# Optimization experiments

Measured on AMD Instinct MI355X. Metric: run time of the kernel, lower is better.

The kernel has to match this reference:

```python
import jax, jax.numpy as jnp
import numpy as np

EMBED_DIM = 1024
NUM_HEADS = 16
HEAD_DIM = EMBED_DIM // NUM_HEADS
B, S = 8, 1024


def setup_inputs() -> dict:
    key = jax.random.key(0)
    ks = jax.random.split(key, 8)
    scale = 1.0 / np.sqrt(EMBED_DIM)
    return {
        "q": jax.random.normal(ks[0], (B, S, EMBED_DIM), jnp.float32),
        "v": jax.random.normal(ks[1], (B, S, EMBED_DIM), jnp.float32),
        "Wq": jax.random.normal(ks[2], (EMBED_DIM, EMBED_DIM), jnp.float32) * scale,
        "bq": jnp.zeros((EMBED_DIM,), jnp.float32),
        "Wk": jax.random.normal(ks[3], (EMBED_DIM, EMBED_DIM), jnp.float32) * scale,
        "bk": jnp.zeros((EMBED_DIM,), jnp.float32),
        "Wv": jax.random.normal(ks[4], (EMBED_DIM, EMBED_DIM), jnp.float32) * scale,
        "bv": jnp.zeros((EMBED_DIM,), jnp.float32),
    }


def reference(q, v, Wq, bq, Wk, bk, Wv, bv):
    # call(q, v, k=None): k defaults to v, then compute_multihead_attention(q, v, k)
    # maps (q_arg=q, k_arg=v, v_arg=v) in self-attention.
    qp = q @ Wq + bq                     # [B, S, E]
    kp = v @ Wk + bk                     # [B, S, E]
    vp = v @ Wv + bv                     # [B, S, E]
    # split along feature dim into heads (same math as tf.split+concat on batch)
    qh = qp.reshape(B, S, NUM_HEADS, HEAD_DIM)
    kh = kp.reshape(B, S, NUM_HEADS, HEAD_DIM)
    vh = vp.reshape(B, S, NUM_HEADS, HEAD_DIM)
    # NOTE: original scales by 1/sqrt(embed_dim), not 1/sqrt(head_dim)
    scores = jnp.einsum("bqhd,bkhd->bhqk", qh, kh) / np.sqrt(EMBED_DIM)
    att = jax.nn.softmax(scores, axis=-1)
    out = jnp.einsum("bhqk,bkhd->bqhd", att, vh)  # [B, S, H, Dh]
    return out.reshape(B, S, EMBED_DIM)
```

## Files before the change

kernel.cpp:

```cpp
#include <hip/hip_runtime.h>
#include <cstdint>
#include <cstddef>

#define E 1024
#define S 1024
#define NB 8
#define NH 16
#define DH 64

typedef __bf16 bf16_t;
typedef __bf16 bf16x8 __attribute__((ext_vector_type(8)));
typedef __bf16 bf16x4 __attribute__((ext_vector_type(4)));
typedef __bf16 bf16x2 __attribute__((ext_vector_type(2)));
typedef short s16x4 __attribute__((ext_vector_type(4)));
typedef float f32x4 __attribute__((ext_vector_type(4)));

static __device__ __forceinline__ void gload_lds16(const void* g, void* l) {
  __builtin_amdgcn_global_load_lds((const __attribute__((address_space(1))) void*)g,
                                   (__attribute__((address_space(3))) void*)l, 16, 0, 0);
}

static __device__ __forceinline__ float fast_exp2(float x) {
#if __has_builtin(__builtin_amdgcn_exp2f)
  return __builtin_amdgcn_exp2f(x);
#else
  float r;
  asm("v_exp_f32 %0, %1" : "=v"(r) : "v"(x));
  return r;
#endif
}

__global__ __launch_bounds__(256) void convert_kernel(
    const float* __restrict__ q, const float* __restrict__ v,
    bf16_t* __restrict__ qb, bf16_t* __restrict__ vb) {
  const float* src = blockIdx.y ? v : q;
  bf16_t* dst = blockIdx.y ? vb : qb;
  const size_t i = ((size_t)blockIdx.x * 256 + threadIdx.x) * 8;
  float4 a = *(const float4*)(src + i);
  float4 b = *(const float4*)(src + i + 4);
  bf16x8 o = {(bf16_t)a.x, (bf16_t)a.y, (bf16_t)a.z, (bf16_t)a.w,
              (bf16_t)b.x, (bf16_t)b.y, (bf16_t)b.z, (bf16_t)b.w};
  *(bf16x8*)(dst + i) = o;
}

__global__ void wtrans_kernel(const float* __restrict__ Wq, const float* __restrict__ Wk,
                              const float* __restrict__ Wv, bf16_t* __restrict__ Wqt,
                              bf16_t* __restrict__ Wkt, bf16_t* __restrict__ Wvt) {
  const float* W = (blockIdx.z == 0) ? Wq : (blockIdx.z == 1) ? Wk : Wv;
  bf16_t* Wt = (blockIdx.z == 0) ? Wqt : (blockIdx.z == 1) ? Wkt : Wvt;
  __shared__ float tile[32][33];
  const int n0 = blockIdx.x * 32, k0 = blockIdx.y * 32;
  const int tx = threadIdx.x, ty = threadIdx.y;
#pragma unroll
  for (int i = ty; i < 32; i += 8)
    tile[i][tx] = W[(size_t)(k0 + i) * E + n0 + tx];
  __syncthreads();
#pragma unroll
  for (int i = ty; i < 32; i += 8)
    Wt[(size_t)(n0 + i) * E + k0 + tx] = (bf16_t)tile[tx][i];
}

__global__ __launch_bounds__(256) void gemm_fused_kernel(
    const bf16_t* __restrict__ qbf, const bf16_t* __restrict__ vbf,
    const bf16_t* __restrict__ Wqt, const bf16_t* __restrict__ Wkt,
    const bf16_t* __restrict__ Wvt, const float* __restrict__ bq,
    const float* __restrict__ bk, const float* __restrict__ bv,
    bf16_t* __restrict__ qp, bf16_t* __restrict__ kp, bf16_t* __restrict__ vp,
    float qscale) {
  __shared__ bf16_t As[128 * 32];
  __shared__ bf16_t Bs[128 * 32];
  const int t = threadIdx.x;
  const int l = t & 63, w = t >> 6;
  const int lc = l & 15, lg = l >> 4;
  const int wm = (w >> 1) * 64, wn = (w & 1) * 64;

  const int nb = blockIdx.y;
  const int sel = nb >> 3;
  const bf16_t* A = sel ? vbf : qbf;
  const bf16_t* Bt = (sel == 0) ? Wqt : (sel == 1) ? Wkt : Wvt;
  const float* bias = (sel == 0) ? bq : (sel == 1) ? bk : bv;
  bf16_t* C = (sel == 0) ? qp : (sel == 1) ? kp : vp;
  const float scale = (sel == 0) ? qscale : 1.0f;

  const int m0 = blockIdx.x * 128;
  const int n0 = (nb & 7) * 128;

  const bf16_t* asrc = A + (size_t)(m0 + (t >> 2)) * E + (t & 3) * 8;
  const bf16_t* bsrc = Bt + (size_t)(n0 + (t >> 2)) * E + (t & 3) * 8;
  char* asd0 = (char*)As + w * 1024;
  char* bsd0 = (char*)Bs + w * 1024;

  f32x4 acc[4][4] = {};

  for (int k0 = 0; k0 < E; k0 += 32) {
    __syncthreads();
    gload_lds16(asrc + k0, asd0);
    gload_lds16(asrc + 64 * E + k0, asd0 + 4096);
    gload_lds16(bsrc + k0, bsd0);
    gload_lds16(bsrc + 64 * E + k0, bsd0 + 4096);
    __syncthreads();

    bf16x8 af[4], bf[4];
#pragma unroll
    for (int mi = 0; mi < 4; ++mi)
      af[mi] = *(const bf16x8*)&As[(wm + mi * 16 + lc) * 32 + lg * 8];
#pragma unroll
    for (int ni = 0; ni < 4; ++ni)
      bf[ni] = *(const bf16x8*)&Bs[(wn + ni * 16 + lc) * 32 + lg * 8];
#pragma unroll
    for (int mi = 0; mi < 4; ++mi)
#pragma unroll
      for (int ni = 0; ni < 4; ++ni)
        acc[mi][ni] = __builtin_amdgcn_mfma_f32_16x16x32_bf16(af[mi], bf[ni], acc[mi][ni], 0, 0, 0);
  }

#pragma unroll
  for (int ni = 0; ni < 4; ++ni) {
    const int n = n0 + wn + ni * 16 + lc;
    const float bv_ = bias[n];
#pragma unroll
    for (int mi = 0; mi < 4; ++mi) {
#pragma unroll
      for (int r = 0; r < 4; ++r) {
        const int m = m0 + wm + mi * 16 + lg * 4 + r;
        C[(size_t)m * E + n] = (bf16_t)((acc[mi][ni][r] + bv_) * scale);
      }
    }
  }
}

#if __has_builtin(__builtin_amdgcn_mfma_f32_16x16x16bf16_1k)
static __device__ __forceinline__ f32x4 mfma16(s16x4 a, s16x4 b, f32x4 c) {
  return __builtin_amdgcn_mfma_f32_16x16x16bf16_1k(a, b, c, 0, 0, 0);
}
#else
static __device__ __forceinline__ f32x4 mfma16(s16x4 a, s16x4 b, f32x4 c) {
  asm volatile("v_mfma_f32_16x16x16_bf16 %0, %1, %2, %0" : "+v"(c) : "v"(a), "v"(b));
  return c;
}
#endif

__global__ __launch_bounds__(256, 2) void attn_kernel(
    const bf16_t* __restrict__ qp, const bf16_t* __restrict__ kp,
    const bf16_t* __restrict__ vp, float* __restrict__ out) {
  __shared__ __align__(16) unsigned char KsB[2][64 * 128];
  __shared__ bf16_t Vs[2][64][72];
  const int t = threadIdx.x;
  const int w = t >> 6, l = t & 63;
  const int lc = l & 15, lg = l >> 4;

  const int swz = (blockIdx.x & 7) * 64 + (blockIdx.x >> 3);
  const int qblk = swz & 3, bh = swz >> 2;
  const int h = bh & 15, b = bh >> 4;
  const int qbase = qblk * 256 + w * 64;
  const size_t bh_off = (size_t)b * S * E + (size_t)h * DH;

  bf16x8 qf[4][2];
#pragma unroll
  for (int qi = 0; qi < 4; ++qi)
#pragma unroll
    for (int kc = 0; kc < 2; ++kc)
      qf[qi][kc] = *(const bf16x8*)(qp + bh_off + (size_t)(qbase + 16 * qi + lc) * E + kc * 32 + lg * 8);

  f32x4 po[4][4] = {};
  float l_[4] = {0.f, 0.f, 0.f, 0.f};

  const int krow = t >> 2, kc4 = t & 3;
  const int vkv2 = (t & 31) * 2, vd0 = (t >> 5) * 8;
  const bf16_t* kbase = kp + bh_off;
  const bf16_t* vbase = vp + bh_off;
  const int ksw = (krow & 7) << 4;

  bf16x8 ka0, ka1, va0, va1;
  {
    const bf16_t* ks = kbase + (size_t)krow * E + kc4 * 16;
    ka0 = *(const bf16x8*)ks;
    ka1 = *(const bf16x8*)(ks + 8);
    const bf16_t* vs = vbase + (size_t)vkv2 * E + vd0;
    va0 = *(const bf16x8*)vs;
    va1 = *(const bf16x8*)(vs + E);
    *(bf16x8*)&KsB[0][krow * 128 + ((kc4 * 32) ^ ksw)] = ka0;
    *(bf16x8*)&KsB[0][krow * 128 + ((kc4 * 32 + 16) ^ ksw)] = ka1;
#pragma unroll
    for (int j = 0; j < 8; ++j) {
      bf16x2 pr;
      pr[0] = va0[j];
      pr[1] = va1[j];
      *(bf16x2*)&Vs[0][vd0 + j][vkv2] = pr;
    }
  }
  int cur = 0;

  for (int kv0 = 0; kv0 < S; kv0 += 64) {
    __syncthreads();

    const bool more = (kv0 + 64 < S);
    if (more) {
      const bf16_t* ks = kbase + (size_t)(kv0 + 64 + krow) * E + kc4 * 16;
      ka0 = *(const bf16x8*)ks;
      ka1 = *(const bf16x8*)(ks + 8);
      const bf16_t* vs = vbase + (size_t)(kv0 + 64 + vkv2) * E + vd0;
      va0 = *(const bf16x8*)vs;
      va1 = *(const bf16x8*)(vs + E);
    }

    s16x4 pa[4][4];
    __builtin_amdgcn_s_setprio(1);
#pragma unroll
    for (int kvb = 0; kvb < 4; ++kvb) {
      const int row = kvb * 16 + lc;
      const int sw = (lc & 7) << 4;
      bf16x8 ak0 = *(const bf16x8*)&KsB[cur][row * 128 + ((lg * 16) ^ sw)];
      bf16x8 ak1 = *(const bf16x8*)&KsB[cur][row * 128 + ((64 + lg * 16) ^ sw)];
      f32x4 sc[4] = {};
#pragma unroll
      for (int qi = 0; qi < 4; ++qi) {
        sc[qi] = __builtin_amdgcn_mfma_f32_16x16x32_bf16(ak0, qf[qi][0], sc[qi], 0, 0, 0);
        sc[qi] = __builtin_amdgcn_mfma_f32_16x16x32_bf16(ak1, qf[qi][1], sc[qi], 0, 0, 0);
      }
#pragma unroll
      for (int qi = 0; qi < 4; ++qi) {
        const float e0 = fast_exp2(sc[qi][0]);
        const float e1 = fast_exp2(sc[qi][1]);
        const float e2 = fast_exp2(sc[qi][2]);
        const float e3 = fast_exp2(sc[qi][3]);
        l_[qi] += (e0 + e1) + (e2 + e3);
        bf16x4 pb = {(bf16_t)e0, (bf16_t)e1, (bf16_t)e2, (bf16_t)e3};
        pa[qi][kvb] = *(s16x4*)&pb;
      }
    }

#pragma unroll
    for (int ki = 0; ki < 4; ++ki) {
      s16x4 av[4];
#pragma unroll
      for (int ni = 0; ni < 4; ++ni)
        av[ni] = *(const s16x4*)&Vs[cur][16 * ni + lc][16 * ki + lg * 4];
#pragma unroll
      for (int qi = 0; qi < 4; ++qi)
#pragma unroll
        for (int ni = 0; ni < 4; ++ni)
          po[qi][ni] = mfma16(av[ni], pa[qi][ki], po[qi][ni]);
    }
    __builtin_amdgcn_s_setprio(0);

    if (more) {
      const int nb_ = cur ^ 1;
      *(bf16x8*)&KsB[nb_][krow * 128 + ((kc4 * 32) ^ ksw)] = ka0;
      *(bf16x8*)&KsB[nb_][krow * 128 + ((kc4 * 32 + 16) ^ ksw)] = ka1;
#pragma unroll
      for (int j = 0; j < 8; ++j) {
        bf16x2 pr;
        pr[0] = va0[j];
        pr[1] = va1[j];
        *(bf16x2*)&Vs[nb_][vd0 + j][vkv2] = pr;
      }
      cur = nb_;
    }
  }

#pragma unroll
  for (int qi = 0; qi < 4; ++qi) {
    float lt = l_[qi];
    lt += __shfl_xor(lt, 16, 64);
    lt += __shfl_xor(lt, 32, 64);
    const float inv = 1.0f / lt;
    const int qrow = qbase + 16 * qi + lc;
    float* op = out + (size_t)b * S * E + (size_t)qrow * E + h * DH;
#pragma unroll
    for (int ni = 0; ni < 4; ++ni) {
      f32x4 r = po[qi][ni] * inv;
      *(f32x4*)(op + 16 * ni + lg * 4) = r;
    }
  }
}

extern "C" void kernel_launch(void* const* d_in, const int* in_sizes, int n_in,
                              void* d_out, int out_size, void* d_ws, size_t ws_size,
                              hipStream_t stream) {
  const float* q  = (const float*)d_in[0];
  const float* v  = (const float*)d_in[1];
  const float* Wq = (const float*)d_in[2];
  const float* bq = (const float*)d_in[3];
  const float* Wk = (const float*)d_in[4];
  const float* bk = (const float*)d_in[5];
  const float* Wv = (const float*)d_in[6];
  const float* bv = (const float*)d_in[7];
  float* out = (float*)d_out;

  char* ws = (char*)d_ws;
  bf16_t* Wqt = (bf16_t*)(ws);
  bf16_t* Wkt = (bf16_t*)(ws + (size_t)2 * 1024 * 1024);
  bf16_t* Wvt = (bf16_t*)(ws + (size_t)4 * 1024 * 1024);
  bf16_t* qp  = (bf16_t*)(ws + (size_t)6 * 1024 * 1024);
  bf16_t* kp  = (bf16_t*)(ws + (size_t)22 * 1024 * 1024);
  bf16_t* vp  = (bf16_t*)(ws + (size_t)38 * 1024 * 1024);

  bf16_t* qbf = (bf16_t*)d_out;
  bf16_t* vbf = qbf + (size_t)NB * S * E;

  convert_kernel<<<dim3(4096, 2), 256, 0, stream>>>(q, v, qbf, vbf);
  wtrans_kernel<<<dim3(32, 32, 3), dim3(32, 8), 0, stream>>>(Wq, Wk, Wv, Wqt, Wkt, Wvt);

  const float qscale = 0.03125f * 1.44269504088896f;
  gemm_fused_kernel<<<dim3(64, 24), 256, 0, stream>>>(qbf, vbf, Wqt, Wkt, Wvt,
                                                      bq, bk, bv, qp, kp, vp, qscale);
  attn_kernel<<<dim3(512), 256, 0, stream>>>(qp, kp, vp, out);
}
```

Baseline: 139.1 us.

## Fuse fp32-to-bf16 input conversion into projection GEMM with register-prefetched A

```diff
diff --git a/kernel.cpp b/kernel.cpp
--- a/kernel.cpp
+++ b/kernel.cpp
@@ -30,19 +30,6 @@
 #endif
 }
 
-__global__ __launch_bounds__(256) void convert_kernel(
-    const float* __restrict__ q, const float* __restrict__ v,
-    bf16_t* __restrict__ qb, bf16_t* __restrict__ vb) {
-  const float* src = blockIdx.y ? v : q;
-  bf16_t* dst = blockIdx.y ? vb : qb;
-  const size_t i = ((size_t)blockIdx.x * 256 + threadIdx.x) * 8;
-  float4 a = *(const float4*)(src + i);
-  float4 b = *(const float4*)(src + i + 4);
-  bf16x8 o = {(bf16_t)a.x, (bf16_t)a.y, (bf16_t)a.z, (bf16_t)a.w,
-              (bf16_t)b.x, (bf16_t)b.y, (bf16_t)b.z, (bf16_t)b.w};
-  *(bf16x8*)(dst + i) = o;
-}
-
 __global__ void wtrans_kernel(const float* __restrict__ Wq, const float* __restrict__ Wk,
                               const float* __restrict__ Wv, bf16_t* __restrict__ Wqt,
                               bf16_t* __restrict__ Wkt, bf16_t* __restrict__ Wvt) {
@@ -61,13 +48,12 @@
 }
 
 __global__ __launch_bounds__(256) void gemm_fused_kernel(
-    const bf16_t* __restrict__ qbf, const bf16_t* __restrict__ vbf,
+    const float* __restrict__ qf32, const float* __restrict__ vf32,
     const bf16_t* __restrict__ Wqt, const bf16_t* __restrict__ Wkt,
     const bf16_t* __restrict__ Wvt, const float* __restrict__ bq,
     const float* __restrict__ bk, const float* __restrict__ bv,
     bf16_t* __restrict__ qp, bf16_t* __restrict__ kp, bf16_t* __restrict__ vp,
     float qscale) {
-  __shared__ bf16_t As[128 * 32];
   __shared__ bf16_t Bs[128 * 32];
   const int t = threadIdx.x;
   const int l = t & 63, w = t >> 6;
@@ -76,7 +62,7 @@
 
   const int nb = blockIdx.y;
   const int sel = nb >> 3;
-  const bf16_t* A = sel ? vbf : qbf;
+  const float* A = sel ? vf32 : qf32;
   const bf16_t* Bt = (sel == 0) ? Wqt : (sel == 1) ? Wkt : Wvt;
   const float* bias = (sel == 0) ? bq : (sel == 1) ? bk : bv;
   bf16_t* C = (sel == 0) ? qp : (sel == 1) ? kp : vp;
@@ -85,34 +71,64 @@
   const int m0 = blockIdx.x * 128;
   const int n0 = (nb & 7) * 128;
 
-  const bf16_t* asrc = A + (size_t)(m0 + (t >> 2)) * E + (t & 3) * 8;
+  const float* arow = A + (size_t)(m0 + wm + lc) * E + lg * 8;
   const bf16_t* bsrc = Bt + (size_t)(n0 + (t >> 2)) * E + (t & 3) * 8;
-  char* asd0 = (char*)As + w * 1024;
   char* bsd0 = (char*)Bs + w * 1024;
 
   f32x4 acc[4][4] = {};
 
-  for (int k0 = 0; k0 < E; k0 += 32) {
-    __syncthreads();
-    gload_lds16(asrc + k0, asd0);
-    gload_lds16(asrc + 64 * E + k0, asd0 + 4096);
+#define LOAD_A(dst, kk)                                   \
+  _Pragma("unroll") for (int mi = 0; mi < 4; ++mi) {      \
+    const float* p_ = arow + (size_t)mi * 16 * E + (kk);  \
+    dst[mi][0] = *(const f32x4*)p_;                       \
+    dst[mi][1] = *(const f32x4*)(p_ + 4);                 \
+  }
+
+#define CVT_A(dst, src)                                                        \
+  _Pragma("unroll") for (int mi = 0; mi < 4; ++mi) {                           \
+    dst[mi] = (bf16x8){(bf16_t)src[mi][0][0], (bf16_t)src[mi][0][1],           \
+                       (bf16_t)src[mi][0][2], (bf16_t)src[mi][0][3],           \
+                       (bf16_t)src[mi][1][0], (bf16_t)src[mi][1][1],           \
+                       (bf16_t)src[mi][1][2], (bf16_t)src[mi][1][3]};          \
+  }
+
+#define DO_MFMA(af_)                                                           \
+  {                                                                            \
+    bf16x8 bf_[4];                                                             \
+    _Pragma("unroll") for (int ni = 0; ni < 4; ++ni)                           \
+      bf_[ni] = *(const bf16x8*)&Bs[(wn + ni * 16 + lc) * 32 + lg * 8];        \
+    _Pragma("unroll") for (int mi = 0; mi < 4; ++mi)                           \
+      _Pragma("unroll") for (int ni = 0; ni < 4; ++ni)                         \
+        acc[mi][ni] =                                                          \
+            __builtin_amdgcn_mfma_f32_16x16x32_bf16(af_[mi], bf_[ni],          \
+                                                    acc[mi][ni], 0, 0, 0);     \
+  }
+
+  f32x4 aA[4][2], aB[4][2];
+  LOAD_A(aA, 0);
+
+  for (int k0 = 0; k0 < E; k0 += 64) {
+    __syncthreads();
     gload_lds16(bsrc + k0, bsd0);
     gload_lds16(bsrc + 64 * E + k0, bsd0 + 4096);
-    __syncthreads();
-
-    bf16x8 af[4], bf[4];
-#pragma unroll
-    for (int mi = 0; mi < 4; ++mi)
-      af[mi] = *(const bf16x8*)&As[(wm + mi * 16 + lc) * 32 + lg * 8];
-#pragma unroll
-    for (int ni = 0; ni < 4; ++ni)
-      bf[ni] = *(const bf16x8*)&Bs[(wn + ni * 16 + lc) * 32 + lg * 8];
-#pragma unroll
-    for (int mi = 0; mi < 4; ++mi)
-#pragma unroll
-      for (int ni = 0; ni < 4; ++ni)
-        acc[mi][ni] = __builtin_amdgcn_mfma_f32_16x16x32_bf16(af[mi], bf[ni], acc[mi][ni], 0, 0, 0);
-  }
+    LOAD_A(aB, k0 + 32);
+    bf16x8 af0[4];
+    CVT_A(af0, aA);
+    __syncthreads();
+    DO_MFMA(af0);
+
+    __syncthreads();
+    gload_lds16(bsrc + k0 + 32, bsd0);
+    gload_lds16(bsrc + 64 * E + k0 + 32, bsd0 + 4096);
+    if (k0 + 64 < E) LOAD_A(aA, k0 + 64);
+    bf16x8 af1[4];
+    CVT_A(af1, aB);
+    __syncthreads();
+    DO_MFMA(af1);
+  }
+#undef LOAD_A
+#undef CVT_A
+#undef DO_MFMA
 
 #pragma unroll
   for (int ni = 0; ni < 4; ++ni) {
@@ -296,14 +312,10 @@
   bf16_t* kp  = (bf16_t*)(ws + (size_t)22 * 1024 * 1024);
   bf16_t* vp  = (bf16_t*)(ws + (size_t)38 * 1024 * 1024);
 
-  bf16_t* qbf = (bf16_t*)d_out;
-  bf16_t* vbf = qbf + (size_t)NB * S * E;
-
-  convert_kernel<<<dim3(4096, 2), 256, 0, stream>>>(q, v, qbf, vbf);
   wtrans_kernel<<<dim3(32, 32, 3), dim3(32, 8), 0, stream>>>(Wq, Wk, Wv, Wqt, Wkt, Wvt);
 
   const float qscale = 0.03125f * 1.44269504088896f;
-  gemm_fused_kernel<<<dim3(64, 24), 256, 0, stream>>>(qbf, vbf, Wqt, Wkt, Wvt,
+  gemm_fused_kernel<<<dim3(64, 24), 256, 0, stream>>>(q, v, Wqt, Wkt, Wvt,
                                                       bq, bk, bv, qp, kp, vp, qscale);
   attn_kernel<<<dim3(512), 256, 0, stream>>>(qp, kp, vp, out);
 }
```

New measurement: 257.0 us. 84.8% more time.

## Rewrite QKV projection GEMM with 256x256 tiles, double-buffered LDS and swizzle

Applied to the files above, without the earlier changes.

```diff
diff --git a/kernel.cpp b/kernel.cpp
--- a/kernel.cpp
+++ b/kernel.cpp
@@ -60,69 +60,133 @@
     Wt[(size_t)(n0 + i) * E + k0 + tx] = (bf16_t)tile[tx][i];
 }
 
-__global__ __launch_bounds__(256) void gemm_fused_kernel(
+__global__ __launch_bounds__(512, 2) void gemm8_kernel(
     const bf16_t* __restrict__ qbf, const bf16_t* __restrict__ vbf,
     const bf16_t* __restrict__ Wqt, const bf16_t* __restrict__ Wkt,
     const bf16_t* __restrict__ Wvt, const float* __restrict__ bq,
     const float* __restrict__ bk, const float* __restrict__ bv,
     bf16_t* __restrict__ qp, bf16_t* __restrict__ kp, bf16_t* __restrict__ vp,
     float qscale) {
-  __shared__ bf16_t As[128 * 32];
-  __shared__ bf16_t Bs[128 * 32];
+  extern __shared__ __align__(16) char smem[];
+
   const int t = threadIdx.x;
-  const int l = t & 63, w = t >> 6;
+  const int wv = t >> 6, l = t & 63;
   const int lc = l & 15, lg = l >> 4;
-  const int wm = (w >> 1) * 64, wn = (w & 1) * 64;
-
-  const int nb = blockIdx.y;
-  const int sel = nb >> 3;
+  const int wr = wv >> 2, wc = wv & 3;
+
+  const int nt = blockIdx.y;
+  const int sel = nt >> 2;
   const bf16_t* A = sel ? vbf : qbf;
   const bf16_t* Bt = (sel == 0) ? Wqt : (sel == 1) ? Wkt : Wvt;
   const float* bias = (sel == 0) ? bq : (sel == 1) ? bk : bv;
   bf16_t* C = (sel == 0) ? qp : (sel == 1) ? kp : vp;
   const float scale = (sel == 0) ? qscale : 1.0f;
 
-  const int m0 = blockIdx.x * 128;
-  const int n0 = (nb & 7) * 128;
-
-  const bf16_t* asrc = A + (size_t)(m0 + (t >> 2)) * E + (t & 3) * 8;
-  const bf16_t* bsrc = Bt + (size_t)(n0 + (t >> 2)) * E + (t & 3) * 8;
-  char* asd0 = (char*)As + w * 1024;
-  char* bsd0 = (char*)Bs + w * 1024;
-
-  f32x4 acc[4][4] = {};
-
-  for (int k0 = 0; k0 < E; k0 += 32) {
-    __syncthreads();
-    gload_lds16(asrc + k0, asd0);
-    gload_lds16(asrc + 64 * E + k0, asd0 + 4096);
-    gload_lds16(bsrc + k0, bsd0);
-    gload_lds16(bsrc + 64 * E + k0, bsd0 + 4096);
-    __syncthreads();
-
-    bf16x8 af[4], bf[4];
-#pragma unroll
-    for (int mi = 0; mi < 4; ++mi)
-      af[mi] = *(const bf16x8*)&As[(wm + mi * 16 + lc) * 32 + lg * 8];
-#pragma unroll
-    for (int ni = 0; ni < 4; ++ni)
-      bf[ni] = *(const bf16x8*)&Bs[(wn + ni * 16 + lc) * 32 + lg * 8];
-#pragma unroll
-    for (int mi = 0; mi < 4; ++mi)
-#pragma unroll
-      for (int ni = 0; ni < 4; ++ni)
-        acc[mi][ni] = __builtin_amdgcn_mfma_f32_16x16x32_bf16(af[mi], bf[ni], acc[mi][ni], 0, 0, 0);
-  }
+  const int m0 = blockIdx.x * 256;
+  const int n0 = (nt & 3) * 256;
+
+  const int srow = t >> 3;
+  const int scol = 8 * ((t & 7) ^ (srow & 7));
+  const bf16_t* aS = A + (size_t)(m0 + srow) * E + scol;
+  const bf16_t* bS = Bt + (size_t)(n0 + srow) * E + scol;
+  char* const aD = smem + wv * 1024;
+  char* const bD = smem + 65536 + wv * 1024;
+
+#define STAGE(tile, buf)                                                     \
+  {                                                                          \
+    const bf16_t* as_ = aS + (tile) * 64;                                    \
+    const bf16_t* bs_ = bS + (tile) * 64;                                    \
+    char* ad_ = aD + (buf) * 32768;                                          \
+    char* bd_ = bD + (buf) * 32768;                                          \
+    _Pragma("unroll") for (int i = 0; i < 4; ++i)                            \
+        gload_lds16(as_ + i * 64 * E, ad_ + i * 8192);                       \
+    _Pragma("unroll") for (int i = 0; i < 4; ++i)                            \
+        gload_lds16(bs_ + i * 64 * E, bd_ + i * 8192);                       \
+  }
+
+  const int arow0 = wr * 128 + lc;
+  const int brow0 = wc * 64 + lc;
+  const int col0 = (lg << 4) ^ ((lc & 7) << 4);
+
+#define RD_A(Ab, mi, ks) (*(const bf16x8*)((Ab) + ((arow0 + (mi) * 16) << 7) + (col0 ^ ((ks) << 6))))
+#define RD_B(Bb, ni, ks) (*(const bf16x8*)((Bb) + ((brow0 + (ni) * 16) << 7) + (col0 ^ ((ks) << 6))))
+
+  f32x4 acc[8][4] = {};
+
+#define MFMA16(afr, bfr, mo, no)                                             \
+  _Pragma("unroll") for (int mi = 0; mi < 4; ++mi)                           \
+      _Pragma("unroll") for (int ni = 0; ni < 2; ++ni)                       \
+          _Pragma("unroll") for (int ks = 0; ks < 2; ++ks)                   \
+              acc[(mo) + mi][(no) + ni] = __builtin_amdgcn_mfma_f32_16x16x32_bf16( \
+                  afr[mi][ks], bfr[ni][ks], acc[(mo) + mi][(no) + ni], 0, 0, 0);
+
+#define BAR() asm volatile("s_barrier" ::: "memory")
+
+#define KTILE(Ab, Bb)                                                        \
+  {                                                                          \
+    bf16x8 fa[4][2], fb[2][2];                                               \
+                                           \
+    _Pragma("unroll") for (int mi = 0; mi < 4; ++mi) {                       \
+      fa[mi][0] = RD_A(Ab, mi, 0); fa[mi][1] = RD_A(Ab, mi, 1); }            \
+    _Pragma("unroll") for (int ni = 0; ni < 2; ++ni) {                       \
+      fb[ni][0] = RD_B(Bb, ni, 0); fb[ni][1] = RD_B(Bb, ni, 1); }            \
+    BAR();                                                                   \
+    __builtin_amdgcn_s_setprio(1); MFMA16(fa, fb, 0, 0);                     \
+    __builtin_amdgcn_s_setprio(0); BAR();                                    \
+                                     \
+    _Pragma("unroll") for (int ni = 0; ni < 2; ++ni) {                       \
+      fb[ni][0] = RD_B(Bb, 2 + ni, 0); fb[ni][1] = RD_B(Bb, 2 + ni, 1); }    \
+    BAR();                                                                   \
+    __builtin_amdgcn_s_setprio(1); MFMA16(fa, fb, 0, 2);                     \
+    __builtin_amdgcn_s_setprio(0); BAR();                                    \
+                                     \
+    _Pragma("unroll") for (int mi = 0; mi < 4; ++mi) {                       \
+      fa[mi][0] = RD_A(Ab, 4 + mi, 0); fa[mi][1] = RD_A(Ab, 4 + mi, 1); }    \
+    BAR();                                                                   \
+    __builtin_amdgcn_s_setprio(1); MFMA16(fa, fb, 4, 2);                     \
+    __builtin_amdgcn_s_setprio(0); BAR();                                    \
+                                  \
+    _Pragma("unroll") for (int ni = 0; ni < 2; ++ni) {                       \
+      fb[ni][0] = RD_B(Bb, ni, 0); fb[ni][1] = RD_B(Bb, ni, 1); }            \
+    BAR();                                                                   \
+    __builtin_amdgcn_s_setprio(1); MFMA16(fa, fb, 4, 0);                     \
+    __builtin_amdgcn_s_setprio(0); BAR();                                    \
+  }
+
+  STAGE(0, 0);
+  STAGE(1, 1);
+  asm volatile("s_waitcnt vmcnt(8)" ::: "memory");
+  BAR();
+
+  for (int tk = 0; tk < 14; ++tk) {
+    char* Ab = smem + (tk & 1) * 32768;
+    char* Bb = smem + 65536 + (tk & 1) * 32768;
+    KTILE(Ab, Bb);
+    STAGE(tk + 2, tk & 1);
+    asm volatile("s_waitcnt vmcnt(8)" ::: "memory");
+    BAR();
+  }
+  KTILE(smem, smem + 65536);
+  asm volatile("s_waitcnt vmcnt(0)" ::: "memory");
+  BAR();
+  KTILE(smem + 32768, smem + 65536 + 32768);
+
+#undef KTILE
+#undef MFMA16
+#undef RD_A
+#undef RD_B
+#undef STAGE
+#undef BAR
 
 #pragma unroll
   for (int ni = 0; ni < 4; ++ni) {
-    const int n = n0 + wn + ni * 16 + lc;
+    const int n = n0 + wc * 64 + ni * 16 + lc;
     const float bv_ = bias[n];
 #pragma unroll
-    for (int mi = 0; mi < 4; ++mi) {
+    for (int mi = 0; mi < 8; ++mi) {
 #pragma unroll
       for (int r = 0; r < 4; ++r) {
-        const int m = m0 + wm + mi * 16 + lg * 4 + r;
+        const int m = m0 + wr * 128 + mi * 16 + lg * 4 + r;
         C[(size_t)m * E + n] = (bf16_t)((acc[mi][ni][r] + bv_) * scale);
       }
     }
@@ -299,11 +363,14 @@
   bf16_t* qbf = (bf16_t*)d_out;
   bf16_t* vbf = qbf + (size_t)NB * S * E;
 
+  (void)hipFuncSetAttribute((const void*)gemm8_kernel,
+                            hipFuncAttributeMaxDynamicSharedMemorySize, 131072);
+
   convert_kernel<<<dim3(4096, 2), 256, 0, stream>>>(q, v, qbf, vbf);
   wtrans_kernel<<<dim3(32, 32, 3), dim3(32, 8), 0, stream>>>(Wq, Wk, Wv, Wqt, Wkt, Wvt);
 
   const float qscale = 0.03125f * 1.44269504088896f;
-  gemm_fused_kernel<<<dim3(64, 24), 256, 0, stream>>>(qbf, vbf, Wqt, Wkt, Wvt,
+  gemm8_kernel<<<dim3(32, 12), 512, 131072, stream>>>(qbf, vbf, Wqt, Wkt, Wvt,
                                                       bq, bk, bv, qp, kp, vp, qscale);
   attn_kernel<<<dim3(512), 256, 0, stream>>>(qp, kp, vp, out);
 }
```

After: 144.8 us. +4.2%, slower.

## Triple-buffer projection GEMM with 128x256 tiles and swizzled LDS

Applied to the files above, without the earlier changes.

```diff
diff --git a/kernel.cpp b/kernel.cpp
--- a/kernel.cpp
+++ b/kernel.cpp
@@ -60,22 +60,22 @@
     Wt[(size_t)(n0 + i) * E + k0 + tx] = (bf16_t)tile[tx][i];
 }
 
-__global__ __launch_bounds__(256) void gemm_fused_kernel(
+__global__ __launch_bounds__(256, 2) void gemm3_kernel(
     const bf16_t* __restrict__ qbf, const bf16_t* __restrict__ vbf,
     const bf16_t* __restrict__ Wqt, const bf16_t* __restrict__ Wkt,
     const bf16_t* __restrict__ Wvt, const float* __restrict__ bq,
     const float* __restrict__ bk, const float* __restrict__ bv,
     bf16_t* __restrict__ qp, bf16_t* __restrict__ kp, bf16_t* __restrict__ vp,
     float qscale) {
-  __shared__ bf16_t As[128 * 32];
-  __shared__ bf16_t Bs[128 * 32];
+  extern __shared__ __align__(16) char smem[];
+
   const int t = threadIdx.x;
-  const int l = t & 63, w = t >> 6;
+  const int wv = t >> 6, l = t & 63;
   const int lc = l & 15, lg = l >> 4;
-  const int wm = (w >> 1) * 64, wn = (w & 1) * 64;
-
-  const int nb = blockIdx.y;
-  const int sel = nb >> 3;
+  const int wc = wv;
+
+  const int nt = blockIdx.y;
+  const int sel = nt >> 2;
   const bf16_t* A = sel ? vbf : qbf;
   const bf16_t* Bt = (sel == 0) ? Wqt : (sel == 1) ? Wkt : Wvt;
   const float* bias = (sel == 0) ? bq : (sel == 1) ? bk : bv;
@@ -83,46 +83,81 @@
   const float scale = (sel == 0) ? qscale : 1.0f;
 
   const int m0 = blockIdx.x * 128;
-  const int n0 = (nb & 7) * 128;
-
-  const bf16_t* asrc = A + (size_t)(m0 + (t >> 2)) * E + (t & 3) * 8;
-  const bf16_t* bsrc = Bt + (size_t)(n0 + (t >> 2)) * E + (t & 3) * 8;
-  char* asd0 = (char*)As + w * 1024;
-  char* bsd0 = (char*)Bs + w * 1024;
-
-  f32x4 acc[4][4] = {};
-
-  for (int k0 = 0; k0 < E; k0 += 32) {
-    __syncthreads();
-    gload_lds16(asrc + k0, asd0);
-    gload_lds16(asrc + 64 * E + k0, asd0 + 4096);
-    gload_lds16(bsrc + k0, bsd0);
-    gload_lds16(bsrc + 64 * E + k0, bsd0 + 4096);
-    __syncthreads();
-
-    bf16x8 af[4], bf[4];
-#pragma unroll
-    for (int mi = 0; mi < 4; ++mi)
-      af[mi] = *(const bf16x8*)&As[(wm + mi * 16 + lc) * 32 + lg * 8];
+  const int n0 = (nt & 3) * 256;
+
+  const int rr = t >> 2;
+  const int sgE = ((((t & 3) + ((t >> 3) & 3)) & 3)) << 3;
+  const bf16_t* aS0 = A + (size_t)(m0 + rr) * E + sgE;
+  const bf16_t* aS1 = A + (size_t)(m0 + 64 + rr) * E + sgE;
+  const bf16_t* bS0 = Bt + (size_t)(n0 + rr) * E + sgE;
+  const bf16_t* bS1 = Bt + (size_t)(n0 + 64 + rr) * E + sgE;
+  const bf16_t* bS2 = Bt + (size_t)(n0 + 128 + rr) * E + sgE;
+  const bf16_t* bS3 = Bt + (size_t)(n0 + 192 + rr) * E + sgE;
+
+#define STAGE(tile, buf)                          \
+  {                                               \
+    const int k0_ = (tile) * 32;                  \
+    char* d_ = smem + (buf) * 24576 + wv * 1024;  \
+    gload_lds16(aS0 + k0_, d_);                   \
+    gload_lds16(aS1 + k0_, d_ + 4096);            \
+    gload_lds16(bS0 + k0_, d_ + 8192);            \
+    gload_lds16(bS1 + k0_, d_ + 12288);           \
+    gload_lds16(bS2 + k0_, d_ + 16384);           \
+    gload_lds16(bS3 + k0_, d_ + 20480);           \
+  }
+
+  const int cRd = ((lg - (lc >> 1)) & 3) << 4;
+  const int aRowB = lc * 64 + cRd;
+  const int bRowB = 8192 + (wc * 64 + lc) * 64 + cRd;
+
+  f32x4 acc[8][4] = {};
+
+  STAGE(0, 0);
+  STAGE(1, 1);
+  asm volatile("s_waitcnt vmcnt(6)" ::: "memory");
+  asm volatile("s_barrier" ::: "memory");
+
+  int bufC = 0, bufS = 2;
+  for (int tk = 0; tk < 32; ++tk) {
+    const char* base = smem + bufC * 24576;
+    if (tk + 2 < 32) STAGE(tk + 2, bufS);
+
+    bf16x8 fa[8], fb[4];
 #pragma unroll
     for (int ni = 0; ni < 4; ++ni)
-      bf[ni] = *(const bf16x8*)&Bs[(wn + ni * 16 + lc) * 32 + lg * 8];
-#pragma unroll
-    for (int mi = 0; mi < 4; ++mi)
+      fb[ni] = *(const bf16x8*)(base + bRowB + ni * 1024);
+#pragma unroll
+    for (int mi = 0; mi < 8; ++mi)
+      fa[mi] = *(const bf16x8*)(base + aRowB + mi * 1024);
+
+    __builtin_amdgcn_s_setprio(1);
+#pragma unroll
+    for (int mi = 0; mi < 8; ++mi)
 #pragma unroll
       for (int ni = 0; ni < 4; ++ni)
-        acc[mi][ni] = __builtin_amdgcn_mfma_f32_16x16x32_bf16(af[mi], bf[ni], acc[mi][ni], 0, 0, 0);
-  }
+        acc[mi][ni] = __builtin_amdgcn_mfma_f32_16x16x32_bf16(fa[mi], fb[ni], acc[mi][ni], 0, 0, 0);
+    __builtin_amdgcn_s_setprio(0);
+
+    if (tk + 2 < 32) {
+      asm volatile("s_waitcnt vmcnt(6)" ::: "memory");
+    } else if (tk == 30) {
+      asm volatile("s_waitcnt vmcnt(0)" ::: "memory");
+    }
+    if (tk < 31) asm volatile("s_barrier" ::: "memory");
+    bufC = (bufC == 2) ? 0 : bufC + 1;
+    bufS = (bufS == 2) ? 0 : bufS + 1;
+  }
+#undef STAGE
 
 #pragma unroll
   for (int ni = 0; ni < 4; ++ni) {
-    const int n = n0 + wn + ni * 16 + lc;
+    const int n = n0 + wc * 64 + ni * 16 + lc;
     const float bv_ = bias[n];
 #pragma unroll
-    for (int mi = 0; mi < 4; ++mi) {
+    for (int mi = 0; mi < 8; ++mi) {
 #pragma unroll
       for (int r = 0; r < 4; ++r) {
-        const int m = m0 + wm + mi * 16 + lg * 4 + r;
+        const int m = m0 + mi * 16 + lg * 4 + r;
         C[(size_t)m * E + n] = (bf16_t)((acc[mi][ni][r] + bv_) * scale);
       }
     }
@@ -299,11 +334,14 @@
   bf16_t* qbf = (bf16_t*)d_out;
   bf16_t* vbf = qbf + (size_t)NB * S * E;
 
+  (void)hipFuncSetAttribute((const void*)gemm3_kernel,
+                            hipFuncAttributeMaxDynamicSharedMemorySize, 73728);
+
   convert_kernel<<<dim3(4096, 2), 256, 0, stream>>>(q, v, qbf, vbf);
   wtrans_kernel<<<dim3(32, 32, 3), dim3(32, 8), 0, stream>>>(Wq, Wk, Wv, Wqt, Wkt, Wvt);
 
   const float qscale = 0.03125f * 1.44269504088896f;
-  gemm_fused_kernel<<<dim3(64, 24), 256, 0, stream>>>(qbf, vbf, Wqt, Wkt, Wvt,
-                                                      bq, bk, bv, qp, kp, vp, qscale);
+  gemm3_kernel<<<dim3(64, 12), 256, 73728, stream>>>(qbf, vbf, Wqt, Wkt, Wvt,
+                                                     bq, bk, bv, qp, kp, vp, qscale);
   attn_kernel<<<dim3(512), 256, 0, stream>>>(qp, kp, vp, out);
 }
```

After: 135.3 us. 2.7% less time.
